# Optimization experiments

Hardware: AMD Instinct MI355X
Metric: run time of the kernel (lower is better)

## Reference

```python
import jax, jax.numpy as jnp
import numpy as np

EPS_ATTN = 1e-5   # LinearCrossAttention eps
EPS_LN = 1e-5     # LayerNorm default eps


def _rot_interleaved(t):
    # rotate_half=False path of timm apply_rot_embed_cat: interleaved pairs
    t1 = t[..., ::2]
    t2 = t[..., 1::2]
    return jnp.stack([-t2, t1], axis=-1).reshape(t.shape)


def _apply_rope_cat(t, rope):
    # rope: [N_r, 2*D] = concat(sin, cos); t: [B, H, N_r, D]
    sin, cos = jnp.split(rope, 2, axis=-1)  # each [N_r, D]
    return t * cos + _rot_interleaved(t) * sin


def _layer_norm(x, g, b):
    m = jnp.mean(x, axis=-1, keepdims=True)
    v = jnp.var(x, axis=-1, keepdims=True)
    return (x - m) * jax.lax.rsqrt(v + EPS_LN) * g + b


def setup_inputs() -> dict:
    key = jax.random.key(0)
    ks = jax.random.split(key, 4)
    B, N, C = 8, 4096, 768
    H, D = 12, 64
    npt = 1
    x = jax.random.normal(ks[0], (B, N, C), dtype=jnp.float32)
    rope = jax.random.normal(ks[1], (N - npt, 2 * D), dtype=jnp.float32)
    qkv_w = jax.random.normal(ks[2], (3 * C, C), dtype=jnp.float32) * (C ** -0.5)
    proj_w = jax.random.normal(ks[3], (C, C), dtype=jnp.float32) * (C ** -0.5)
    return {
        "x": x,
        "rope": rope,
        "qkv_w": qkv_w,
        "q_bias": jnp.zeros((C,), jnp.float32),
        "v_bias": jnp.zeros((C,), jnp.float32),
        "norm_g": jnp.ones((C,), jnp.float32),
        "norm_b": jnp.zeros((C,), jnp.float32),
        "proj_w": proj_w,
        "proj_b": jnp.zeros((C,), jnp.float32),
        "num_heads": 12,
        "num_prefix_tokens": 1,
    }


def reference(x, rope, qkv_w, q_bias, v_bias, norm_g, norm_b, proj_w, proj_b,
              num_heads, num_prefix_tokens):
    B, N, C = x.shape
    H = num_heads
    D = C // H
    npt = num_prefix_tokens

    # fused qkv projection; k_bias is a zero buffer
    qkv_bias = jnp.concatenate([q_bias, jnp.zeros_like(q_bias), v_bias])
    qkv = x @ qkv_w.T + qkv_bias                      # [B, N, 3C]
    qkv = qkv.reshape(B, N, 3, H, D).transpose(2, 0, 3, 1, 4)  # [3, B, H, N, D]
    q, k, v = qkv[0], qkv[1], qkv[2]

    # RoPE on non-prefix tokens
    q = jnp.concatenate([q[:, :, :npt], _apply_rope_cat(q[:, :, npt:], rope)], axis=2)
    k = jnp.concatenate([k[:, :, :npt], _apply_rope_cat(k[:, :, npt:], rope)], axis=2)

    # linear cross-attention with tied softmax feature map
    phi_q = jax.nn.softmax(q, axis=-1)                # [B, H, N, D]
    phi_k = jax.nn.softmax(k, axis=-1)                # [B, H, N, D]
    kv = jnp.einsum('bhnd,bhne->bhde', phi_k, v)      # [B, H, D, D]
    z = jnp.einsum('bhnd,bhd->bhn', phi_q, phi_k.sum(axis=2))  # [B, H, N]
    out = jnp.einsum('bhnd,bhde->bhne', phi_q, kv) / (z[..., None] + EPS_ATTN)

    out = out.transpose(0, 2, 1, 3).reshape(B, N, C)  # [B, N, C]
    out = _layer_norm(out, norm_g, norm_b)            # scale_norm
    out = out @ proj_w.T + proj_b
    return out
```

## Files before the change

### kernel.cpp

```cpp
#include <hip/hip_runtime.h>
#include <stdint.h>


typedef __attribute__((ext_vector_type(8))) short short8;
typedef __attribute__((ext_vector_type(4))) float floatx4;

#define SPLIT_A 16
#define TILES_PER_BLK (32 / SPLIT_A)

__device__ __forceinline__ float b2f(unsigned short u) {
  union { unsigned int i; float f; } v; v.i = ((unsigned int)u) << 16; return v.f;
}
__device__ __forceinline__ unsigned short f2b(float f) {
  union { float f; unsigned int i; } v; v.f = f;
  unsigned int i = v.i;
  unsigned int r = (i + 0x7FFFu + ((i >> 16) & 1u)) >> 16;
  return (unsigned short)r;
}
__device__ __forceinline__ void unpack2(unsigned int u, float& a, float& b) {
  union { unsigned int i; float f; } x, y;
  x.i = u << 16; y.i = u & 0xFFFF0000u;
  a = x.f; b = y.f;
}

__device__ __forceinline__ void stage16(const void* g, void* l) {
#if defined(__has_builtin) && __has_builtin(__builtin_amdgcn_global_load_lds)
  __builtin_amdgcn_global_load_lds(
      (const __attribute__((address_space(1))) unsigned int*)g,
      (__attribute__((address_space(3))) unsigned int*)l, 16, 0, 0);
#else
  *(uint4*)l = *(const uint4*)g;
#endif
}

__global__ __launch_bounds__(256) void f32_to_bf16(
    const float* __restrict__ in, unsigned short* __restrict__ out, int n) {
  const int i = (blockIdx.x * 256 + threadIdx.x) * 8;
  if (i + 7 < n) {
    float4 a = *(const float4*)(in + i);
    float4 b = *(const float4*)(in + i + 4);
    unsigned short tmp[8] = {f2b(a.x), f2b(a.y), f2b(a.z), f2b(a.w),
                             f2b(b.x), f2b(b.y), f2b(b.z), f2b(b.w)};
    *(uint4*)(out + i) = *(uint4*)tmp;
  }
}

__global__ __launch_bounds__(256) void prep(
    const float* __restrict__ w, const float* __restrict__ pw,
    const float* __restrict__ qb, const float* __restrict__ vb,
    const float* __restrict__ pb,
    unsigned short* __restrict__ wbf, unsigned short* __restrict__ pwbf,
    float* __restrict__ qkvb, float* __restrict__ projb) {
  const int blk = blockIdx.x, t = threadIdx.x;
  if (blk < 1152) {
    const float* src = (blk < 864) ? w : pw;
    unsigned short* dst = (blk < 864) ? wbf : pwbf;
    const int i = ((blk < 864 ? blk : blk - 864) * 256 + t) * 8;
    float4 a = *(const float4*)(src + i);
    float4 b = *(const float4*)(src + i + 4);
    unsigned short tmp[8] = {f2b(a.x), f2b(a.y), f2b(a.z), f2b(a.w),
                             f2b(b.x), f2b(b.y), f2b(b.z), f2b(b.w)};
    *(uint4*)(dst + i) = *(uint4*)tmp;
  } else {
    const int i = (blk - 1152) * 256 + t;
    if (i < 2304) qkvb[i] = (i < 768) ? qb[i] : (i >= 1536 ? vb[i - 1536] : 0.f);
    if (i < 768) projb[i] = pb[i];
  }
}

template <int OUT_BF16>
__global__ __launch_bounds__(256) void gemm_bt(
    const unsigned short* __restrict__ A, const unsigned short* __restrict__ W,
    const float* __restrict__ bias, void* __restrict__ Out,
    int M, int K, int Nout, int nbn) {
  __shared__ __align__(16) unsigned short sA[128 * 32];
  __shared__ __align__(16) unsigned short sB[128 * 32];
  const int nwg = gridDim.x;
  const int orig = blockIdx.x;
  const int wg = (orig & 7) * (nwg >> 3) + (orig >> 3);
  const int bm = wg / nbn;
  const int bn = wg - bm * nbn;
  const int t = threadIdx.x;
  const int lane = t & 63, wave = t >> 6;
  const int wm = (wave >> 1) * 64, wn = (wave & 1) * 64;
  const int lr = t >> 2;
  const int lc = (t & 3) * 8;
  const size_t baseA = (size_t)(bm * 128 + lr) * K + lc;
  const size_t baseB = (size_t)(bn * 128 + lr) * K + lc;
  floatx4 acc[4][4] = {};

  const int mr = lane & 15, kq = (lane >> 4) * 8;
  for (int k0 = 0; k0 < K; k0 += 32) {
    stage16(A + baseA + k0, &sA[t * 8]);
    stage16(A + baseA + (size_t)64 * K + k0, &sA[2048 + t * 8]);
    stage16(W + baseB + k0, &sB[t * 8]);
    stage16(W + baseB + (size_t)64 * K + k0, &sB[2048 + t * 8]);
    __syncthreads();
    short8 af[4], bfr[4];
#pragma unroll
    for (int i = 0; i < 4; i++) af[i] = *(const short8*)&sA[(wm + i * 16 + mr) * 32 + kq];
#pragma unroll
    for (int j = 0; j < 4; j++) bfr[j] = *(const short8*)&sB[(wn + j * 16 + mr) * 32 + kq];
#pragma unroll
    for (int i = 0; i < 4; i++)
#pragma unroll
      for (int j = 0; j < 4; j++)
        acc[i][j] = __builtin_amdgcn_mfma_f32_16x16x32_bf16(af[i], bfr[j], acc[i][j], 0, 0, 0);
    __syncthreads();
  }

  const int mr4 = (lane >> 4) * 4, nc = lane & 15;
#pragma unroll
  for (int j = 0; j < 4; j++) {
    const int gc = bn * 128 + wn + j * 16 + nc;
    const float bv = bias[gc];
#pragma unroll
    for (int i = 0; i < 4; i++) {
      const int gr0 = bm * 128 + wm + i * 16 + mr4;
#pragma unroll
      for (int r = 0; r < 4; r++) {
        float v = acc[i][j][r] + bv;
        if (OUT_BF16)
          ((unsigned short*)Out)[(size_t)(gr0 + r) * Nout + gc] = f2b(v);
        else
          ((float*)Out)[(size_t)(gr0 + r) * Nout + gc] = v;
      }
    }
  }
}

__global__ __launch_bounds__(256) void pass_a(
    const unsigned short* __restrict__ qkv, const float* __restrict__ rope,
    float* __restrict__ kvP) {
  __shared__ float sphi[128 * 65];
  __shared__ __align__(16) unsigned short sv[128 * 64];
  const int bh = blockIdx.x, b = bh / 12, h = bh % 12;
  const int sp = blockIdx.y;
  const int t = threadIdx.x;
  const int lane = t & 63, wave = t >> 6;
  const int dg = lane >> 2;
  const int eg = lane & 3;
  float acc[4][16] = {};
  float ks4[4] = {};

  const int tile0 = sp * TILES_PER_BLK;
  for (int tile = tile0; tile < tile0 + TILES_PER_BLK; tile++) {
    __syncthreads();
    if (t < 128) {
      const int n = tile * 128 + t;
      const size_t rowb = (size_t)(b * 4096 + n) * 2304;
      const unsigned short* kp = qkv + rowb + 768 + h * 64;
      float kk[64];
#pragma unroll
      for (int c = 0; c < 8; c++) {
        uint4 u = *(const uint4*)(kp + c * 8);
        unpack2(u.x, kk[c * 8 + 0], kk[c * 8 + 1]);
        unpack2(u.y, kk[c * 8 + 2], kk[c * 8 + 3]);
        unpack2(u.z, kk[c * 8 + 4], kk[c * 8 + 5]);
        unpack2(u.w, kk[c * 8 + 6], kk[c * 8 + 7]);
      }
      if (n > 0) {
        const float* rp = rope + (size_t)(n - 1) * 128;
#pragma unroll
        for (int c = 0; c < 8; c++) {
          float sn[8], cs[8];
          *(float4*)&sn[0] = *(const float4*)(rp + c * 8);
          *(float4*)&sn[4] = *(const float4*)(rp + c * 8 + 4);
          *(float4*)&cs[0] = *(const float4*)(rp + 64 + c * 8);
          *(float4*)&cs[4] = *(const float4*)(rp + 64 + c * 8 + 4);
#pragma unroll
          for (int i = 0; i < 4; i++) {
            float e = kk[c * 8 + 2 * i], o = kk[c * 8 + 2 * i + 1];
            kk[c * 8 + 2 * i] = e * cs[2 * i] - o * sn[2 * i];
            kk[c * 8 + 2 * i + 1] = o * cs[2 * i + 1] + e * sn[2 * i + 1];
          }
        }
      }
      float mx = kk[0];
#pragma unroll
      for (int i = 1; i < 64; i++) mx = fmaxf(mx, kk[i]);
      float s = 0.f;
#pragma unroll
      for (int i = 0; i < 64; i++) { float e = __expf(kk[i] - mx); kk[i] = e; s += e; }
      const float inv = 1.f / s;
#pragma unroll
      for (int d = 0; d < 64; d++) sphi[t * 65 + d] = kk[d] * inv;
      const unsigned short* vp = qkv + rowb + 1536 + h * 64;
#pragma unroll
      for (int c = 0; c < 8; c++)
        *(uint4*)&sv[t * 64 + c * 8] = *(const uint4*)(vp + c * 8);
    }
    __syncthreads();
    const int n0 = wave * 32;
    for (int nn = n0; nn < n0 + 32; nn++) {
      float p[4];
#pragma unroll
      for (int i = 0; i < 4; i++) p[i] = sphi[nn * 65 + dg * 4 + i];
#pragma unroll
      for (int i = 0; i < 4; i++) ks4[i] += p[i];
      float vv[16];
      {
        uint4 u0 = *(const uint4*)&sv[nn * 64 + eg * 16];
        uint4 u1 = *(const uint4*)&sv[nn * 64 + eg * 16 + 8];
        unpack2(u0.x, vv[0], vv[1]);   unpack2(u0.y, vv[2], vv[3]);
        unpack2(u0.z, vv[4], vv[5]);   unpack2(u0.w, vv[6], vv[7]);
        unpack2(u1.x, vv[8], vv[9]);   unpack2(u1.y, vv[10], vv[11]);
        unpack2(u1.z, vv[12], vv[13]); unpack2(u1.w, vv[14], vv[15]);
      }
#pragma unroll
      for (int i = 0; i < 4; i++)
#pragma unroll
        for (int j = 0; j < 16; j++)
          acc[i][j] += p[i] * vv[j];
    }
  }

  __syncthreads();
  float* sred = sphi;
  float* o = kvP + ((size_t)bh * SPLIT_A + sp) * 4160;
#pragma unroll
  for (int half = 0; half < 2; half++) {
    if (wave != 0) {
      float* row = &sred[((wave - 1) * 64 + lane) * 33];
#pragma unroll
      for (int i = 0; i < 4; i++)
#pragma unroll
        for (int jj = 0; jj < 8; jj++) row[i * 8 + jj] = acc[i][half * 8 + jj];
    }
    __syncthreads();
    if (wave == 0) {
#pragma unroll
      for (int jj = 0; jj < 8; jj++) {
        float4 s4;
        float sv4[4];
#pragma unroll
        for (int i = 0; i < 4; i++) {
          float s = acc[i][half * 8 + jj];
#pragma unroll
          for (int w = 0; w < 3; w++) s += sred[(w * 64 + lane) * 33 + i * 8 + jj];
          sv4[i] = s;
        }
        s4.x = sv4[0]; s4.y = sv4[1]; s4.z = sv4[2]; s4.w = sv4[3];
        const int e = eg * 16 + half * 8 + jj;
        *(float4*)&o[e * 64 + dg * 4] = s4;
      }
    }
    __syncthreads();
  }
  if (wave != 0) {
#pragma unroll
    for (int i = 0; i < 4; i++) sred[((wave - 1) * 64 + lane) * 5 + i] = ks4[i];
  }
  __syncthreads();
  if (wave == 0 && eg == 0) {
    float4 s4;
    float sv4[4];
#pragma unroll
    for (int i = 0; i < 4; i++) {
      float s = ks4[i];
#pragma unroll
      for (int w = 0; w < 3; w++) s += sred[(w * 64 + lane) * 5 + i];
      sv4[i] = s;
    }
    s4.x = sv4[0]; s4.y = sv4[1]; s4.z = sv4[2]; s4.w = sv4[3];
    *(float4*)&o[4096 + dg * 4] = s4;
  }
}

__global__ __launch_bounds__(256) void reduce_kv(
    const float* __restrict__ kvP, float* __restrict__ kvG) {
  const int i = blockIdx.x * 256 + threadIdx.x;
  if (i >= 96 * 4160) return;
  const int bh = i / 4160, r = i - bh * 4160;
  const float* p = kvP + (size_t)bh * SPLIT_A * 4160 + r;
  float s = 0.f;
#pragma unroll
  for (int sp = 0; sp < SPLIT_A; sp++) s += p[(size_t)sp * 4160];
  kvG[i] = s;
}

__global__ __launch_bounds__(256) void pass_b(
    const unsigned short* __restrict__ qkv, const float* __restrict__ rope,
    const float* __restrict__ kvG, unsigned short* __restrict__ attn) {
  __shared__ __align__(16) unsigned short sp_[256 * 64];
  __shared__ __align__(16) unsigned short skv[64 * 64];
  __shared__ float szi[256];
  __shared__ float sks[64];
  const int bh = blockIdx.x, b = bh / 12, h = bh % 12;
  const int t = threadIdx.x;
  const float* kvb = kvG + (size_t)bh * 4160;

  {
    const int e = t >> 2, q = t & 3;
    const float* src = kvb + e * 64 + q * 16;
    unsigned short tmp[16];
#pragma unroll
    for (int i = 0; i < 16; i++) tmp[i] = f2b(src[i]);
    *(uint4*)&skv[e * 64 + (((q * 2) ^ (e & 7)) * 8)] = *(uint4*)&tmp[0];
    *(uint4*)&skv[e * 64 + (((q * 2 + 1) ^ (e & 7)) * 8)] = *(uint4*)&tmp[8];
  }
  if (t < 64) sks[t] = kvb[4096 + t];
  __syncthreads();

  const int n = blockIdx.y * 256 + t;
  const size_t rowb = (size_t)(b * 4096 + n) * 2304;
  const unsigned short* qp = qkv + rowb + h * 64;
  float ph[64];
#pragma unroll
  for (int c = 0; c < 8; c++) {
    uint4 u = *(const uint4*)(qp + c * 8);
    unpack2(u.x, ph[c * 8 + 0], ph[c * 8 + 1]);
    unpack2(u.y, ph[c * 8 + 2], ph[c * 8 + 3]);
    unpack2(u.z, ph[c * 8 + 4], ph[c * 8 + 5]);
    unpack2(u.w, ph[c * 8 + 6], ph[c * 8 + 7]);
  }
  if (n > 0) {
    const float* rp = rope + (size_t)(n - 1) * 128;
#pragma unroll
    for (int c = 0; c < 8; c++) {
      float sn[8], cs[8];
      *(float4*)&sn[0] = *(const float4*)(rp + c * 8);
      *(float4*)&sn[4] = *(const float4*)(rp + c * 8 + 4);
      *(float4*)&cs[0] = *(const float4*)(rp + 64 + c * 8);
      *(float4*)&cs[4] = *(const float4*)(rp + 64 + c * 8 + 4);
#pragma unroll
      for (int i = 0; i < 4; i++) {
        float e = ph[c * 8 + 2 * i], o = ph[c * 8 + 2 * i + 1];
        ph[c * 8 + 2 * i] = e * cs[2 * i] - o * sn[2 * i];
        ph[c * 8 + 2 * i + 1] = o * cs[2 * i + 1] + e * sn[2 * i + 1];
      }
    }
  }
  float mx = ph[0];
#pragma unroll
  for (int i = 1; i < 64; i++) mx = fmaxf(mx, ph[i]);
  float s = 0.f;
#pragma unroll
  for (int i = 0; i < 64; i++) { float e = __expf(ph[i] - mx); ph[i] = e; s += e; }
  const float inv = 1.f / s;
  float z = 0.f;
#pragma unroll
  for (int i = 0; i < 64; i++) { ph[i] *= inv; z += ph[i] * sks[i]; }
  szi[t] = 1.f / (z + 1e-5f);

#pragma unroll
  for (int sl = 0; sl < 8; sl += 2) {
    unsigned short tmp[16];
#pragma unroll
    for (int i = 0; i < 16; i++) tmp[i] = f2b(ph[sl * 8 + i]);
    *(uint4*)&sp_[t * 64 + ((sl ^ (t & 7)) * 8)] = *(uint4*)&tmp[0];
    *(uint4*)&sp_[t * 64 + (((sl + 1) ^ (t & 7)) * 8)] = *(uint4*)&tmp[8];
  }
  __syncthreads();

  const int lane = t & 63, wv = t >> 6;
  const int fr = lane & 15, fq = lane >> 4;
  floatx4 acc[4][4] = {};
#pragma unroll
  for (int kk = 0; kk < 2; kk++) {
    short8 kvf[4], pf[4];
#pragma unroll
    for (int j = 0; j < 4; j++) {
      const int e = j * 16 + fr;
      kvf[j] = *(const short8*)&skv[e * 64 + (((kk * 4 + fq) ^ (e & 7)) * 8)];
    }
#pragma unroll
    for (int i = 0; i < 4; i++) {
      const int tok = wv * 64 + i * 16 + fr;
      pf[i] = *(const short8*)&sp_[tok * 64 + (((kk * 4 + fq) ^ (tok & 7)) * 8)];
    }
#pragma unroll
    for (int i = 0; i < 4; i++)
#pragma unroll
      for (int j = 0; j < 4; j++)
        acc[i][j] = __builtin_amdgcn_mfma_f32_16x16x32_bf16(kvf[j], pf[i], acc[i][j], 0, 0, 0);
  }

#pragma unroll
  for (int i = 0; i < 4; i++) {
    const int tokl = wv * 64 + i * 16 + fr;
    const float zi = szi[tokl];
    unsigned short* orow =
        attn + (size_t)(b * 4096 + blockIdx.y * 256 + tokl) * 768 + h * 64;
#pragma unroll
    for (int j = 0; j < 4; j++) {
      const int e0 = j * 16 + fq * 4;
      unsigned short pk[4] = {f2b(acc[i][j][0] * zi), f2b(acc[i][j][1] * zi),
                              f2b(acc[i][j][2] * zi), f2b(acc[i][j][3] * zi)};
      *(uint2*)(orow + e0) = *(const uint2*)pk;
    }
  }
}

__global__ __launch_bounds__(256) void ln_kernel(
    unsigned short* __restrict__ buf, const float* __restrict__ g,
    const float* __restrict__ be) {
  const int row = blockIdx.x;
  const int t = threadIdx.x;
  unsigned short* p = buf + (size_t)row * 768;
  const float x0 = b2f(p[t]), x1 = b2f(p[t + 256]), x2 = b2f(p[t + 512]);
  float s = x0 + x1 + x2;
  float ss = x0 * x0 + x1 * x1 + x2 * x2;
#pragma unroll
  for (int m = 1; m < 64; m <<= 1) { s += __shfl_xor(s, m); ss += __shfl_xor(ss, m); }
  __shared__ float red[8];
  const int wave = t >> 6, lane = t & 63;
  if (lane == 0) { red[wave] = s; red[4 + wave] = ss; }
  __syncthreads();
  s = red[0] + red[1] + red[2] + red[3];
  ss = red[4] + red[5] + red[6] + red[7];
  const float mean = s * (1.f / 768.f);
  const float var = ss * (1.f / 768.f) - mean * mean;
  const float rsq = rsqrtf(var + 1e-5f);
  p[t] = f2b((x0 - mean) * rsq * g[t] + be[t]);
  p[t + 256] = f2b((x1 - mean) * rsq * g[t + 256] + be[t + 256]);
  p[t + 512] = f2b((x2 - mean) * rsq * g[t + 512] + be[t + 512]);
}

extern "C" void kernel_launch(void* const* d_in, const int* in_sizes, int n_in,
                              void* d_out, int out_size, void* d_ws, size_t ws_size,
                              hipStream_t stream) {
  (void)in_sizes; (void)n_in; (void)out_size; (void)ws_size;
  const float* x      = (const float*)d_in[0];
  const float* rope   = (const float*)d_in[1];
  const float* qkv_w  = (const float*)d_in[2];
  const float* q_bias = (const float*)d_in[3];
  const float* v_bias = (const float*)d_in[4];
  const float* norm_g = (const float*)d_in[5];
  const float* norm_b = (const float*)d_in[6];
  const float* proj_w = (const float*)d_in[7];
  const float* proj_b = (const float*)d_in[8];

  char* ws = (char*)d_ws;
  unsigned short* qkv  = (unsigned short*)ws;
  unsigned short* attn = (unsigned short*)(ws + 150994944);
  unsigned short* xbf  = attn;
  float* kvP   = (float*)(ws + 150994944);
  float* kvG   = (float*)(ws + 201326592);
  float* qkvb  = (float*)(ws + 202924032);
  float* projb = (float*)(ws + 202933248);
  unsigned short* wbf  = (unsigned short*)(ws + 202936320);
  unsigned short* pwbf = (unsigned short*)(ws + 206475264);

  f32_to_bf16<<<dim3(12288), dim3(256), 0, stream>>>(x, xbf, 25165824);
  prep<<<dim3(1161), dim3(256), 0, stream>>>(qkv_w, proj_w, q_bias, v_bias,
                                             proj_b, wbf, pwbf, qkvb, projb);
  gemm_bt<1><<<dim3(4608), dim3(256), 0, stream>>>(xbf, wbf, qkvb, qkv, 32768, 768, 2304, 18);
  pass_a<<<dim3(96, SPLIT_A), dim3(256), 0, stream>>>(qkv, rope, kvP);
  reduce_kv<<<dim3(1560), dim3(256), 0, stream>>>(kvP, kvG);
  pass_b<<<dim3(96, 16), dim3(256), 0, stream>>>(qkv, rope, kvG, attn);
  ln_kernel<<<dim3(32768), dim3(256), 0, stream>>>(attn, norm_g, norm_b);
  gemm_bt<0><<<dim3(1536), dim3(256), 0, stream>>>(attn, pwbf, projb, d_out, 32768, 768, 768, 6);
}
```

Baseline: 583.3 us.

## Replace 128x128 GEMM with 256x256 double-buffered, swizzled, 8-wave pipelined GEMM

Measured after the change: 594.0 us. Within noise of the previous version (+1.8%).

```diff
diff --git a/kernel.cpp b/kernel.cpp
--- a/kernel.cpp
+++ b/kernel.cpp
@@ -7,6 +7,11 @@
 
 #define SPLIT_A 16
 #define TILES_PER_BLK (32 / SPLIT_A)
+
+#define SBAR()  do { asm volatile("" ::: "memory"); __builtin_amdgcn_s_barrier(); asm volatile("" ::: "memory"); } while (0)
+#define LGKM0() do { asm volatile("s_waitcnt lgkmcnt(0)" ::: "memory"); __builtin_amdgcn_sched_barrier(0); } while (0)
+#define WAITV6() asm volatile("s_waitcnt vmcnt(6)" ::: "memory")
+#define WAITV0() asm volatile("s_waitcnt vmcnt(0)" ::: "memory")
 
 __device__ __forceinline__ float b2f(unsigned short u) {
   union { unsigned int i; float f; } v; v.i = ((unsigned int)u) << 16; return v.f;
@@ -69,54 +74,134 @@
 }
 
 template <int OUT_BF16>
-__global__ __launch_bounds__(256) void gemm_bt(
+__global__ __launch_bounds__(512, 2) void gemm256(
     const unsigned short* __restrict__ A, const unsigned short* __restrict__ W,
     const float* __restrict__ bias, void* __restrict__ Out,
-    int M, int K, int Nout, int nbn) {
-  __shared__ __align__(16) unsigned short sA[128 * 32];
-  __shared__ __align__(16) unsigned short sB[128 * 32];
+    int K, int Nout, int nbn, int NT) {
+  extern __shared__ __align__(16) unsigned short lds[];
   const int nwg = gridDim.x;
   const int orig = blockIdx.x;
   const int wg = (orig & 7) * (nwg >> 3) + (orig >> 3);
-  const int bm = wg / nbn;
-  const int bn = wg - bm * nbn;
+  const int bm = wg / nbn, bn = wg - bm * nbn;
   const int t = threadIdx.x;
   const int lane = t & 63, wave = t >> 6;
-  const int wm = (wave >> 1) * 64, wn = (wave & 1) * 64;
-  const int lr = t >> 2;
-  const int lc = (t & 3) * 8;
-  const size_t baseA = (size_t)(bm * 128 + lr) * K + lc;
-  const size_t baseB = (size_t)(bn * 128 + lr) * K + lc;
-  floatx4 acc[4][4] = {};
-
-  const int mr = lane & 15, kq = (lane >> 4) * 8;
-  for (int k0 = 0; k0 < K; k0 += 32) {
-    stage16(A + baseA + k0, &sA[t * 8]);
-    stage16(A + baseA + (size_t)64 * K + k0, &sA[2048 + t * 8]);
-    stage16(W + baseB + k0, &sB[t * 8]);
-    stage16(W + baseB + (size_t)64 * K + k0, &sB[2048 + t * 8]);
-    __syncthreads();
-    short8 af[4], bfr[4];
-#pragma unroll
-    for (int i = 0; i < 4; i++) af[i] = *(const short8*)&sA[(wm + i * 16 + mr) * 32 + kq];
-#pragma unroll
-    for (int j = 0; j < 4; j++) bfr[j] = *(const short8*)&sB[(wn + j * 16 + mr) * 32 + kq];
-#pragma unroll
-    for (int i = 0; i < 4; i++)
-#pragma unroll
-      for (int j = 0; j < 4; j++)
-        acc[i][j] = __builtin_amdgcn_mfma_f32_16x16x32_bf16(af[i], bfr[j], acc[i][j], 0, 0, 0);
-    __syncthreads();
+  const int wr = wave >> 2, wc = wave & 3;
+  const int mr = lane & 15, kq8 = lane >> 4;
+
+  const int rh0 = t >> 3, sl0 = t & 7;
+  const size_t growA = (size_t)bm * 256;
+  const size_t growB = (size_t)bn * 256;
+
+  #define STAGE_HALF(buf, op, G, grow, k0, half)                               \
+    do {                                                                       \
+      const int row0_ = (half)*128 + rh0;                                      \
+      const int row1_ = row0_ + 64;                                            \
+      const unsigned short* s0_ =                                              \
+          (G) + ((grow) + row0_) * (size_t)K + (k0) + ((sl0 ^ (row0_ & 7)) * 8);\
+      const unsigned short* s1_ =                                              \
+          (G) + ((grow) + row1_) * (size_t)K + (k0) + ((sl0 ^ (row1_ & 7)) * 8);\
+      unsigned short* d0_ = lds + (buf)*32768 + (op)*16384 + (half)*8192 + t*8;\
+      stage16(s0_, d0_);                                                       \
+      stage16(s1_, d0_ + 4096);                                                \
+    } while (0)
+
+  floatx4 acc[8][4] = {};
+  short8 afr[4][2], bfr[4][2];
+
+  #define RD_A(buf, i, kk)                                                     \
+    (*(const short8*)&lds[(buf)*32768 + (wr*128 + (i)*16 + mr)*64 +            \
+        ((((kk)*4 + kq8) ^ ((wr*128 + (i)*16 + mr) & 7)) * 8)])
+  #define RD_B(buf, j, kk)                                                     \
+    (*(const short8*)&lds[(buf)*32768 + 16384 + (wc*64 + (j)*16 + mr)*64 +     \
+        ((((kk)*4 + kq8) ^ ((wc*64 + (j)*16 + mr) & 7)) * 8)])
+
+  #define QUAD(ih, jh)                                                         \
+    do {                                                                       \
+      __builtin_amdgcn_s_setprio(1);                                           \
+      _Pragma("unroll")                                                        \
+      for (int i_ = 0; i_ < 4; i_++)                                           \
+        _Pragma("unroll")                                                      \
+        for (int jr_ = 0; jr_ < 2; jr_++)                                      \
+          _Pragma("unroll")                                                    \
+          for (int kk_ = 0; kk_ < 2; kk_++)                                    \
+            acc[(ih)*4 + i_][(jh)*2 + jr_] =                                   \
+                __builtin_amdgcn_mfma_f32_16x16x32_bf16(                       \
+                    afr[i_][kk_], bfr[(jh)*2 + jr_][kk_],                      \
+                    acc[(ih)*4 + i_][(jh)*2 + jr_], 0, 0, 0);                  \
+      __builtin_amdgcn_s_setprio(0);                                           \
+    } while (0)
+
+  STAGE_HALF(0, 0, A, growA, 0, 0);
+  STAGE_HALF(0, 0, A, growA, 0, 1);
+  STAGE_HALF(0, 1, W, growB, 0, 0);
+  STAGE_HALF(0, 1, W, growB, 0, 1);
+  STAGE_HALF(1, 1, W, growB, 64, 0);
+  STAGE_HALF(1, 1, W, growB, 64, 1);
+  STAGE_HALF(1, 0, A, growA, 64, 0);
+  WAITV6();
+  SBAR();
+
+  const int NI = NT >> 1;
+  for (int it = 0; it < NI; ++it) {
+    const int ta = 2 * it, tb = ta + 1;
+    const int kA = (ta + 2) * 64, kB = (tb + 2) * 64;
+    const bool gA = (ta + 2) < NT, gB = (tb + 2) < NT;
+#pragma unroll
+    for (int i = 0; i < 4; i++) { afr[i][0] = RD_A(0, i, 0); afr[i][1] = RD_A(0, i, 1); }
+#pragma unroll
+    for (int j = 0; j < 4; j++) { bfr[j][0] = RD_B(0, j, 0); bfr[j][1] = RD_B(0, j, 1); }
+    STAGE_HALF(1, 0, A, growA, tb * 64, 1);
+    SBAR(); LGKM0();
+    QUAD(0, 0);
+    SBAR();
+    if (gA) STAGE_HALF(0, 1, W, growB, kA, 0);
+    SBAR();
+    QUAD(0, 1);
+    SBAR();
+#pragma unroll
+    for (int i = 0; i < 4; i++) { afr[i][0] = RD_A(0, i + 4, 0); afr[i][1] = RD_A(0, i + 4, 1); }
+    if (gA) STAGE_HALF(0, 1, W, growB, kA, 1);
+    SBAR(); LGKM0();
+    QUAD(1, 0);
+    SBAR();
+    if (gA) STAGE_HALF(0, 0, A, growA, kA, 0);
+    SBAR();
+    QUAD(1, 1);
+    if (gA) WAITV6(); else WAITV0();
+    SBAR();
+#pragma unroll
+    for (int i = 0; i < 4; i++) { afr[i][0] = RD_A(1, i, 0); afr[i][1] = RD_A(1, i, 1); }
+#pragma unroll
+    for (int j = 0; j < 4; j++) { bfr[j][0] = RD_B(1, j, 0); bfr[j][1] = RD_B(1, j, 1); }
+    if (gA) STAGE_HALF(0, 0, A, growA, kA, 1);
+    SBAR(); LGKM0();
+    QUAD(0, 0);
+    SBAR();
+    if (gB) STAGE_HALF(1, 1, W, growB, kB, 0);
+    SBAR();
+    QUAD(0, 1);
+    SBAR();
+#pragma unroll
+    for (int i = 0; i < 4; i++) { afr[i][0] = RD_A(1, i + 4, 0); afr[i][1] = RD_A(1, i + 4, 1); }
+    if (gB) STAGE_HALF(1, 1, W, growB, kB, 1);
+    SBAR(); LGKM0();
+    QUAD(1, 0);
+    SBAR();
+    if (gB) STAGE_HALF(1, 0, A, growA, kB, 0);
+    SBAR();
+    QUAD(1, 1);
+    if (gB) WAITV6(); else WAITV0();
+    SBAR();
   }
 
   const int mr4 = (lane >> 4) * 4, nc = lane & 15;
 #pragma unroll
   for (int j = 0; j < 4; j++) {
-    const int gc = bn * 128 + wn + j * 16 + nc;
+    const int gc = bn * 256 + wc * 64 + j * 16 + nc;
     const float bv = bias[gc];
 #pragma unroll
-    for (int i = 0; i < 4; i++) {
-      const int gr0 = bm * 128 + wm + i * 16 + mr4;
+    for (int i = 0; i < 8; i++) {
+      const int gr0 = bm * 256 + wr * 128 + i * 16 + mr4;
 #pragma unroll
       for (int r = 0; r < 4; r++) {
         float v = acc[i][j][r] + bv;
@@ -127,6 +212,10 @@
       }
     }
   }
+  #undef STAGE_HALF
+  #undef RD_A
+  #undef RD_B
+  #undef QUAD
 }
 
 __global__ __launch_bounds__(256) void pass_a(
@@ -442,13 +531,20 @@
   unsigned short* wbf  = (unsigned short*)(ws + 202936320);
   unsigned short* pwbf = (unsigned short*)(ws + 206475264);
 
+  hipFuncSetAttribute(reinterpret_cast<const void*>(&gemm256<1>),
+                      hipFuncAttributeMaxDynamicSharedMemorySize, 131072);
+  hipFuncSetAttribute(reinterpret_cast<const void*>(&gemm256<0>),
+                      hipFuncAttributeMaxDynamicSharedMemorySize, 131072);
+
   f32_to_bf16<<<dim3(12288), dim3(256), 0, stream>>>(x, xbf, 25165824);
   prep<<<dim3(1161), dim3(256), 0, stream>>>(qkv_w, proj_w, q_bias, v_bias,
                                              proj_b, wbf, pwbf, qkvb, projb);
-  gemm_bt<1><<<dim3(4608), dim3(256), 0, stream>>>(xbf, wbf, qkvb, qkv, 32768, 768, 2304, 18);
+  gemm256<1><<<dim3(1152), dim3(512), 131072, stream>>>(xbf, wbf, qkvb, qkv,
+                                                        768, 2304, 9, 12);
   pass_a<<<dim3(96, SPLIT_A), dim3(256), 0, stream>>>(qkv, rope, kvP);
   reduce_kv<<<dim3(1560), dim3(256), 0, stream>>>(kvP, kvG);
   pass_b<<<dim3(96, 16), dim3(256), 0, stream>>>(qkv, rope, kvG, attn);
   ln_kernel<<<dim3(32768), dim3(256), 0, stream>>>(attn, norm_g, norm_b);
-  gemm_bt<0><<<dim3(1536), dim3(256), 0, stream>>>(attn, pwbf, projb, d_out, 32768, 768, 768, 6);
-}
+  gemm256<0><<<dim3(384), dim3(512), 131072, stream>>>(attn, pwbf, projb, d_out,
+                                                       768, 768, 3, 12);
+}
```
